# Performance work log

Hardware: AMD Instinct MI355X
Metric: run time of the kernel (lower is better)

Reference implementation:

```python
import jax, jax.numpy as jnp
import numpy as np

N_NODES = 10000
N_EDGES = 80000
IN_DIM, HID, OUT_DIM, HEADS = 768, 512, 768, 4
NEG_SLOPE = 0.2


def setup_inputs() -> dict:
    key = jax.random.key(0)
    ks = jax.random.split(key, 10)
    g = 0.05
    return {
        "x": jax.random.normal(ks[0], (N_NODES, IN_DIM), jnp.float32),
        "edge_index": jax.random.randint(ks[1], (2, N_EDGES), 0, N_NODES, jnp.int64),
        # layer 1: GATConv(768 -> 512, heads=4, concat=True)
        "W1": jax.random.normal(ks[2], (IN_DIM, HEADS * HID), jnp.float32) * g,
        "a1_src": jax.random.normal(ks[3], (HEADS, HID), jnp.float32) * g,
        "a1_dst": jax.random.normal(ks[4], (HEADS, HID), jnp.float32) * g,
        "b1": jnp.zeros((HEADS * HID,), jnp.float32),
        # layer 2: GATConv(2048 -> 768, heads=1, concat=False)
        "W2": jax.random.normal(ks[5], (HEADS * HID, OUT_DIM), jnp.float32) * g,
        "a2_src": jax.random.normal(ks[6], (1, OUT_DIM), jnp.float32) * g,
        "a2_dst": jax.random.normal(ks[7], (1, OUT_DIM), jnp.float32) * g,
        "b2": jnp.zeros((OUT_DIM,), jnp.float32),
    }


def _gat_layer(x, src, dst, W, a_src, a_dst, b, heads, d_out, concat):
    N = x.shape[0]
    h = (x @ W).reshape(N, heads, d_out)              # [N, H, D]
    as_n = jnp.einsum('nhd,hd->nh', h, a_src)          # [N, H]
    ad_n = jnp.einsum('nhd,hd->nh', h, a_dst)
    e = jax.nn.leaky_relu(as_n[src] + ad_n[dst], NEG_SLOPE)  # [E, H]
    # segment softmax over destination nodes
    e_max = jax.lax.stop_gradient(jax.ops.segment_max(e, dst, num_segments=N))
    ex = jnp.exp(e - e_max[dst])
    denom = jax.ops.segment_sum(ex, dst, num_segments=N)
    alpha = ex / (denom[dst] + 1e-16)                  # [E, H]
    msg = alpha[:, :, None] * h[src]                   # [E, H, D]
    out = jax.ops.segment_sum(msg, dst, num_segments=N)  # [N, H, D]
    out = out.reshape(N, heads * d_out) if concat else out.mean(axis=1)
    return out + b


def reference(x, edge_index, W1, a1_src, a1_dst, b1, W2, a2_src, a2_dst, b2):
    N = x.shape[0]
    # PyG GATConv default: add self-loops
    loops = jnp.arange(N, dtype=edge_index.dtype)
    src = jnp.concatenate([edge_index[0], loops])
    dst = jnp.concatenate([edge_index[1], loops])
    h = _gat_layer(x, src, dst, W1, a1_src, a1_dst, b1, HEADS, HID, True)
    h = jax.nn.elu(h)
    out = _gat_layer(h, src, dst, W2, a2_src, a2_dst, b2, 1, OUT_DIM, False)
    return out
```

## Files before the change

### kernel.cpp

```cpp
#include <hip/hip_runtime.h>
#include <hip/hip_bf16.h>

#define N_NODES 10000
#define E_REAL  80000
#define E_TOTAL 90000
#define IN_DIM  768
#define HID     512
#define HEADS   4
#define OUT_DIM 768
#define HD1     (HEADS * HID)
#define NEG_SLOPE 0.2f
#define H1_HSTRIDE (N_NODES * HID)

typedef unsigned short ushort_t;
typedef unsigned int uint_t;

__device__ inline float b2f(ushort_t u) { return __uint_as_float(((uint_t)u) << 16); }
__device__ inline ushort_t f2b(float f) {
    __hip_bfloat16 h = __float2bfloat16(f);
    return *reinterpret_cast<ushort_t*>(&h);
}

__device__ inline void edge_sd(const int* __restrict__ ei, int e, int& s, int& d) {
    if (e < E_REAL) { s = ei[e]; d = ei[E_REAL + e]; }
    else            { s = e - E_REAL; d = s; }
}

#define GLDS(g, l) __builtin_amdgcn_global_load_lds( \
    (const __attribute__((address_space(1))) void*)(g), \
    (__attribute__((address_space(3))) void*)(l), 16, 0, 0)

static const long B_H1B  = 0L;
static const long B_HB   = 40960000L;
static const long B_XB   = 81920000L;
static const long B_W1T  = 97280000L;
static const long B_W2T  = 100425728L;
static const long B_SM   = 103571456L;
static const long SM_AS1   = 0;
static const long SM_AD1   = 40000;
static const long SM_AS2   = 80000;
static const long SM_AD2   = 90000;
static const long SM_CNT   = 100000;
static const long SM_ROWS  = 110000;
static const long SM_CURS  = 120016;
static const long SM_END   = 130016;
static const long B_CSRS = B_SM + SM_END * 4;

__global__ __launch_bounds__(256)
void cast_bf16(const float* __restrict__ in, ushort_t* __restrict__ o, long n) {
    long i = ((long)blockIdx.x * 256 + threadIdx.x) * 8;
    if (i >= n) return;
    float4 v0 = *(const float4*)(in + i);
    float4 v1 = *(const float4*)(in + i + 4);
    ushort_t r[8] = {f2b(v0.x), f2b(v0.y), f2b(v0.z), f2b(v0.w),
                     f2b(v1.x), f2b(v1.y), f2b(v1.z), f2b(v1.w)};
    *(uint4*)(o + i) = *(uint4*)r;
}

__global__ __launch_bounds__(256)
void cast_transpose(const float* __restrict__ W, ushort_t* __restrict__ WT,
                    int K, int N) {
    __shared__ ushort_t t[32][33];
    const int n0 = blockIdx.x * 32, k0 = blockIdx.y * 32;
    const int tx = threadIdx.x & 31, ty = threadIdx.x >> 5;
#pragma unroll
    for (int i = 0; i < 4; ++i) {
        int k = ty + i * 8;
        t[k][tx] = f2b(W[(long)(k0 + k) * N + n0 + tx]);
    }
    __syncthreads();
#pragma unroll
    for (int i = 0; i < 4; ++i) {
        int n = ty + i * 8;
        WT[(long)(n0 + n) * K + k0 + tx] = t[tx][n];
    }
}

typedef short bf16x8 __attribute__((ext_vector_type(8)));
typedef float f32x4 __attribute__((ext_vector_type(4)));

#define GBM 256
#define GBN 128
#define GBK 64
#define ABUF (GBM * GBK)
#define BBUF (GBN * GBK)
#define GEMM_LDS_BYTES ((3 * (ABUF + BBUF)) * 2)

template<int CMODE>
__global__ __launch_bounds__(512)
void gemm8p(const ushort_t* __restrict__ A, const ushort_t* __restrict__ BT,
            ushort_t* __restrict__ C, int M, int N, int K) {
    extern __shared__ ushort_t sm_[];
    ushort_t* smA = sm_;
    ushort_t* smB = sm_ + 3 * ABUF;
    const int tid  = threadIdx.x;
    const int wave = tid >> 6, lane = tid & 63;
    const int quad = lane >> 4, l16 = lane & 15;
    const int bm = blockIdx.y * GBM, bn = blockIdx.x * GBN;
    const int wr = (wave >> 1) * 64, wc = (wave & 1) * 64;
    const int NT = K / GBK;

    const int  rA  = tid >> 3;
    const long cs8 = (long)(((tid & 7) ^ ((tid >> 3) & 7)) * 8);
    const ushort_t* aSrc = A  + (long)(bm + rA) * K + cs8;
    const ushort_t* bSrc = BT + (long)(bn + rA) * K + cs8;

    const int aRd  = (wr + l16) * GBK;
    const int bRd  = (wc + l16) * GBK;
    const int swz8 = l16 & 7;
    const int chq0 = ((quad)     ^ swz8) * 8;
    const int chq1 = ((4 + quad) ^ swz8) * 8;

    f32x4 acc[4][4] = {};

#pragma unroll
    for (int tt = 0; tt < 2; ++tt) {
        const long kt = (long)tt * GBK;
#pragma unroll
        for (int i = 0; i < 4; ++i)
            GLDS(aSrc + (long)i * 64 * K + kt,
                 smA + tt * ABUF + (i * 512 + wave * 64) * 8);
#pragma unroll
        for (int i = 0; i < 2; ++i)
            GLDS(bSrc + (long)i * 64 * K + kt,
                 smB + tt * BBUF + (i * 512 + wave * 64) * 8);
    }
    asm volatile("s_waitcnt vmcnt(6)" ::: "memory");
    __builtin_amdgcn_s_barrier();
    __builtin_amdgcn_sched_barrier(0);

    int bc = 0, bnx = 1, bs = 2;
    for (int t = 0; t < NT; ++t) {
        const int offA = bc * ABUF, offB = bc * BBUF;
        const bool stage = (t + 2 < NT);
        const long kt2 = (long)(t + 2) * GBK;
        bf16x8 bfr[2][4], af[2][2];

#pragma unroll
        for (int j = 0; j < 4; ++j) {
            bfr[0][j] = *(const bf16x8*)(smB + offB + bRd + j * 1024 + chq0);
            bfr[1][j] = *(const bf16x8*)(smB + offB + bRd + j * 1024 + chq1);
        }
#pragma unroll
        for (int ii = 0; ii < 2; ++ii) {
            af[0][ii] = *(const bf16x8*)(smA + offA + aRd + ii * 1024 + chq0);
            af[1][ii] = *(const bf16x8*)(smA + offA + aRd + ii * 1024 + chq1);
        }
        if (stage) {
            GLDS(aSrc + kt2,                    smA + bs * ABUF + (wave * 64) * 8);
            GLDS(aSrc + (long)1 * 64 * K + kt2, smA + bs * ABUF + (512 + wave * 64) * 8);
            GLDS(aSrc + (long)2 * 64 * K + kt2, smA + bs * ABUF + (1024 + wave * 64) * 8);
        }
        __builtin_amdgcn_sched_barrier(0);
        __builtin_amdgcn_s_barrier();
        __builtin_amdgcn_sched_barrier(0);
        __builtin_amdgcn_s_setprio(1);
#pragma unroll
        for (int kk = 0; kk < 2; ++kk)
#pragma unroll
            for (int ii = 0; ii < 2; ++ii)
#pragma unroll
                for (int j = 0; j < 4; ++j)
                    acc[ii][j] = __builtin_amdgcn_mfma_f32_16x16x32_bf16(
                        af[kk][ii], bfr[kk][j], acc[ii][j], 0, 0, 0);
        __builtin_amdgcn_s_setprio(0);
        __builtin_amdgcn_sched_barrier(0);
        __builtin_amdgcn_s_barrier();
        __builtin_amdgcn_sched_barrier(0);

#pragma unroll
        for (int ii = 0; ii < 2; ++ii) {
            af[0][ii] = *(const bf16x8*)(smA + offA + aRd + (2 + ii) * 1024 + chq0);
            af[1][ii] = *(const bf16x8*)(smA + offA + aRd + (2 + ii) * 1024 + chq1);
        }
        if (stage) {
            GLDS(aSrc + (long)3 * 64 * K + kt2, smA + bs * ABUF + (1536 + wave * 64) * 8);
            GLDS(bSrc + kt2,                    smB + bs * BBUF + (wave * 64) * 8);
            GLDS(bSrc + (long)1 * 64 * K + kt2, smB + bs * BBUF + (512 + wave * 64) * 8);
        }
        if (stage)             { asm volatile("s_waitcnt vmcnt(6)" ::: "memory"); }
        else if (t + 1 < NT)   { asm volatile("s_waitcnt vmcnt(0)" ::: "memory"); }
        __builtin_amdgcn_sched_barrier(0);
        __builtin_amdgcn_s_barrier();
        __builtin_amdgcn_sched_barrier(0);
        __builtin_amdgcn_s_setprio(1);
#pragma unroll
        for (int kk = 0; kk < 2; ++kk)
#pragma unroll
            for (int ii = 0; ii < 2; ++ii)
#pragma unroll
                for (int j = 0; j < 4; ++j)
                    acc[2 + ii][j] = __builtin_amdgcn_mfma_f32_16x16x32_bf16(
                        af[kk][ii], bfr[kk][j], acc[2 + ii][j], 0, 0, 0);
        __builtin_amdgcn_s_setprio(0);
        __builtin_amdgcn_sched_barrier(0);
        __builtin_amdgcn_s_barrier();
        __builtin_amdgcn_sched_barrier(0);

        int tmp = bc; bc = bnx; bnx = bs; bs = tmp;
    }

#pragma unroll
    for (int i = 0; i < 4; ++i) {
#pragma unroll
        for (int r = 0; r < 4; ++r) {
            int row = bm + wr + i * 16 + quad * 4 + r;
            if (row >= M) continue;
#pragma unroll
            for (int j = 0; j < 4; ++j) {
                int col = bn + wc + j * 16 + l16;
                if (CMODE == 0) {
                    C[(long)row * N + col] = f2b(acc[i][j][r]);
                } else {
                    C[(long)(col >> 9) * H1_HSTRIDE + (long)row * HID + (col & 511)]
                        = f2b(acc[i][j][r]);
                }
            }
        }
    }
}

__global__ __launch_bounds__(256)
void attn1(const ushort_t* __restrict__ h, const float* __restrict__ a_s,
           const float* __restrict__ a_d, float* __restrict__ os,
           float* __restrict__ od) {
    const int n = blockIdx.x;
    const int w = threadIdx.x >> 6, lane = threadIdx.x & 63;
    uint4 hv = *(const uint4*)(h + (long)w * H1_HSTRIDE + (long)n * HID + lane * 8);
    const float* asp = a_s + w * HID + lane * 8;
    const float* adp = a_d + w * HID + lane * 8;
    const ushort_t* pb = (const ushort_t*)&hv;
    float ps = 0.f, pd = 0.f;
#pragma unroll
    for (int c = 0; c < 8; ++c) {
        float v = b2f(pb[c]);
        ps += v * asp[c];
        pd += v * adp[c];
    }
#pragma unroll
    for (int off = 32; off > 0; off >>= 1) {
        ps += __shfl_down(ps, off);
        pd += __shfl_down(pd, off);
    }
    if (lane == 0) { os[n * HEADS + w] = ps; od[n * HEADS + w] = pd; }
}

__global__ __launch_bounds__(256)
void attn2(const ushort_t* __restrict__ h, const float* __restrict__ a_s,
           const float* __restrict__ a_d, float* __restrict__ os,
           float* __restrict__ od) {
    __shared__ float rs[4], rd[4];
    const int n = blockIdx.x, tid = threadIdx.x;
    const int w = tid >> 6, lane = tid & 63;
    float ps = 0.f, pd = 0.f;
#pragma unroll
    for (int j = 0; j < 3; ++j) {
        int c = tid + j * 256;
        float v = b2f(h[(long)n * OUT_DIM + c]);
        ps += v * a_s[c];
        pd += v * a_d[c];
    }
#pragma unroll
    for (int off = 32; off > 0; off >>= 1) {
        ps += __shfl_down(ps, off);
        pd += __shfl_down(pd, off);
    }
    if (lane == 0) { rs[w] = ps; rd[w] = pd; }
    __syncthreads();
    if (tid == 0) {
        os[n] = rs[0] + rs[1] + rs[2] + rs[3];
        od[n] = rd[0] + rd[1] + rd[2] + rd[3];
    }
}

__global__ __launch_bounds__(256)
void hist_dst(const int* __restrict__ ei, int* __restrict__ cnt) {
    int e = blockIdx.x * 256 + threadIdx.x;
    if (e >= E_TOTAL) return;
    int s, d; edge_sd(ei, e, s, d);
    atomicAdd(&cnt[d], 1);
}

#define SCAN_CH 40
__global__ __launch_bounds__(256)
void scan_nodes(const int* __restrict__ cnt, int* __restrict__ rows,
                int* __restrict__ curs) {
    __shared__ int part[256];
    const int tid = threadIdx.x;
    const int base = tid * SCAN_CH;
    int local[SCAN_CH];
    int sum = 0;
#pragma unroll
    for (int i = 0; i < SCAN_CH; ++i) {
        int idx = base + i;
        int v = (idx < N_NODES) ? cnt[idx] : 0;
        local[i] = v; sum += v;
    }
    part[tid] = sum;
    __syncthreads();
    for (int off = 1; off < 256; off <<= 1) {
        int v = (tid >= off) ? part[tid - off] : 0;
        __syncthreads();
        part[tid] += v;
        __syncthreads();
    }
    int run = part[tid] - sum;
#pragma unroll
    for (int i = 0; i < SCAN_CH; ++i) {
        int idx = base + i;
        if (idx < N_NODES) { rows[idx] = run; curs[idx] = run; run += local[i]; }
    }
    if (tid == 255) rows[N_NODES] = run;
}

__global__ __launch_bounds__(256)
void scatter_edges(const int* __restrict__ ei, int* __restrict__ curs,
                   int* __restrict__ csr_src) {
    int e = blockIdx.x * 256 + threadIdx.x;
    if (e >= E_TOTAL) return;
    int s, d; edge_sd(ei, e, s, d);
    int pos = atomicAdd(&curs[d], 1);
    csr_src[pos] = s;
}

__global__ __launch_bounds__(64)
void agg1(const int* __restrict__ rows, const int* __restrict__ csr_src,
          const float* __restrict__ as_n, const float* __restrict__ ad_n,
          const ushort_t* __restrict__ hf, const float* __restrict__ b1,
          ushort_t* __restrict__ o) {
    const int id = blockIdx.x;
    const int g = id & 7, j = id >> 3;
    const int hh = g >> 1;
    const int n = j * 2 + (g & 1);
    const int lane = threadIdx.x;
    const int beg = rows[n], end = rows[n + 1];
    const ushort_t* hsl = hf + (long)hh * H1_HSTRIDE;
    const float adv = ad_n[(long)n * HEADS + hh];
    float acc[8] = {};
    float dsum = 0.f;
    for (int k = beg; k < end; k += 4) {
        int nk = end - k; if (nk > 4) nk = 4;
        uint4 v[4]; float ex[4];
#pragma unroll
        for (int u = 0; u < 4; ++u) {
            if (u < nk) {
                int s = csr_src[k + u];
                float sc = as_n[(long)s * HEADS + hh] + adv;
                sc = sc > 0.f ? sc : NEG_SLOPE * sc;
                ex[u] = __expf(sc);
                v[u]  = *(const uint4*)(hsl + (long)s * HID + lane * 8);
            }
        }
#pragma unroll
        for (int u = 0; u < 4; ++u) {
            if (u < nk) {
                dsum += ex[u];
                const ushort_t* p = (const ushort_t*)&v[u];
#pragma unroll
                for (int c = 0; c < 8; ++c) acc[c] += ex[u] * b2f(p[c]);
            }
        }
    }
    const float dinv = 1.f / (dsum + 1e-16f);
    const float* bp = b1 + hh * HID + lane * 8;
    ushort_t r[8];
#pragma unroll
    for (int c = 0; c < 8; ++c) {
        float vv = acc[c] * dinv + bp[c];
        r[c] = f2b(vv > 0.f ? vv : expm1f(vv));
    }
    *(uint4*)(o + (long)n * HD1 + hh * HID + lane * 8) = *(uint4*)r;
}

#define PF2 8
__global__ __launch_bounds__(256)
void agg2(const int* __restrict__ rows, const int* __restrict__ csr_src,
          const float* __restrict__ as_n, const float* __restrict__ ad_n,
          const ushort_t* __restrict__ hf, const float* __restrict__ b2,
          float* __restrict__ out) {
    const int n = blockIdx.x * 4 + (threadIdx.x >> 6);
    const int lane = threadIdx.x & 63;
    const int beg = rows[n], end = rows[n + 1];
    const float adv = ad_n[n];
    float acc[12] = {};
    float dsum = 0.f;
    for (int k = beg; k < end; k += PF2) {
        int nk = end - k; if (nk > PF2) nk = PF2;
        int sv[PF2];
#pragma unroll
        for (int u = 0; u < PF2; ++u)
            if (u < nk) sv[u] = csr_src[k + u];
        uint4 v4[PF2]; uint2 v2[PF2]; float ex[PF2];
#pragma unroll
        for (int u = 0; u < PF2; ++u) {
            if (u < nk) {
                float sc = as_n[sv[u]] + adv;
                sc = sc > 0.f ? sc : NEG_SLOPE * sc;
                ex[u] = __expf(sc);
                const ushort_t* hp = hf + (long)sv[u] * OUT_DIM;
                v4[u] = *(const uint4*)(hp + lane * 8);
                v2[u] = *(const uint2*)(hp + 512 + lane * 4);
            }
        }
#pragma unroll
        for (int u = 0; u < PF2; ++u) {
            if (u < nk) {
                dsum += ex[u];
                const ushort_t* p4 = (const ushort_t*)&v4[u];
                const ushort_t* p2 = (const ushort_t*)&v2[u];
#pragma unroll
                for (int c = 0; c < 8; ++c) acc[c] += ex[u] * b2f(p4[c]);
#pragma unroll
                for (int c = 0; c < 4; ++c) acc[8 + c] += ex[u] * b2f(p2[c]);
            }
        }
    }
    const float dinv = 1.f / (dsum + 1e-16f);
    float* op = out + (long)n * OUT_DIM;
#pragma unroll
    for (int c = 0; c < 8; ++c)
        op[lane * 8 + c] = acc[c] * dinv + b2[lane * 8 + c];
#pragma unroll
    for (int c = 0; c < 4; ++c)
        op[512 + lane * 4 + c] = acc[8 + c] * dinv + b2[512 + lane * 4 + c];
}

extern "C" void kernel_launch(void* const* d_in, const int* in_sizes, int n_in,
                              void* d_out, int out_size, void* d_ws, size_t ws_size,
                              hipStream_t stream) {
    const float* x   = (const float*)d_in[0];
    const int*   ei  = (const int*)d_in[1];
    const float* W1  = (const float*)d_in[2];
    const float* a1s = (const float*)d_in[3];
    const float* a1d = (const float*)d_in[4];
    const float* b1  = (const float*)d_in[5];
    const float* W2  = (const float*)d_in[6];
    const float* a2s = (const float*)d_in[7];
    const float* a2d = (const float*)d_in[8];
    const float* b2  = (const float*)d_in[9];
    float* out = (float*)d_out;
    char* base = (char*)d_ws;

    ushort_t* h1b = (ushort_t*)(base + B_H1B);
    ushort_t* hb  = (ushort_t*)(base + B_HB);
    ushort_t* xb  = (ushort_t*)(base + B_XB);
    ushort_t* h2b = xb;
    ushort_t* w1t = (ushort_t*)(base + B_W1T);
    ushort_t* w2t = (ushort_t*)(base + B_W2T);
    float*    sm  = (float*)(base + B_SM);

    float* as1  = sm + SM_AS1;
    float* ad1  = sm + SM_AD1;
    float* as2  = sm + SM_AS2;
    float* ad2  = sm + SM_AD2;
    int* cnt    = (int*)(sm + SM_CNT);
    int* rows   = (int*)(sm + SM_ROWS);
    int* curs   = (int*)(sm + SM_CURS);
    int* csr_src = (int*)(base + B_CSRS);

    hipMemsetAsync(cnt, 0, 10000 * sizeof(int), stream);

    {
        long nx = (long)N_NODES * IN_DIM;
        cast_bf16<<<(int)(nx / 8 / 256 + 1), 256, 0, stream>>>(x, xb, nx);
        cast_transpose<<<dim3(HD1 / 32, IN_DIM / 32), 256, 0, stream>>>(W1, w1t, IN_DIM, HD1);
        cast_transpose<<<dim3(OUT_DIM / 32, HD1 / 32), 256, 0, stream>>>(W2, w2t, HD1, OUT_DIM);
        hist_dst<<<(E_TOTAL + 255) / 256, 256, 0, stream>>>(ei, cnt);
        scan_nodes<<<1, 256, 0, stream>>>(cnt, rows, curs);
        scatter_edges<<<(E_TOTAL + 255) / 256, 256, 0, stream>>>(ei, curs, csr_src);
    }

    gemm8p<1><<<dim3(HD1 / GBN, (N_NODES + GBM - 1) / GBM), 512, GEMM_LDS_BYTES, stream>>>(
        xb, w1t, h1b, N_NODES, HD1, IN_DIM);
    attn1<<<N_NODES, 256, 0, stream>>>(h1b, a1s, a1d, as1, ad1);
    agg1<<<N_NODES * HEADS, 64, 0, stream>>>(
        rows, csr_src, as1, ad1, h1b, b1, hb);

    gemm8p<0><<<dim3(OUT_DIM / GBN, (N_NODES + GBM - 1) / GBM), 512, GEMM_LDS_BYTES, stream>>>(
        hb, w2t, h2b, N_NODES, OUT_DIM, HD1);
    attn2<<<N_NODES, 256, 0, stream>>>(h2b, a2s, a2d, as2, ad2);
    agg2<<<N_NODES / 4, 256, 0, stream>>>(
        rows, csr_src, as2, ad2, h2b, b2, out);
}
```

Before: 326.5 us.

## Split layer-1 features into 256-wide slices and double agg1 parallelism

The layer-1 GEMM now writes its output as eight 256-column slices instead of four 512-column head planes. attn1 reads from the new layout, and agg1 launches one 64-thread block per node and slice, so each lane handles 4 features with 8-byte loads. The aim is more blocks in flight to hide gather latency, plus smaller contiguous gathers per slice. The cost is that every edge's score, exponential and index load are now computed twice per head, and each load is narrower.

After: 333.2 us. +2.0%, slower.

```diff
diff --git a/kernel.cpp b/kernel.cpp
--- a/kernel.cpp
+++ b/kernel.cpp
@@ -10,7 +10,7 @@
 #define OUT_DIM 768
 #define HD1     (HEADS * HID)
 #define NEG_SLOPE 0.2f
-#define H1_HSTRIDE (N_NODES * HID)
+#define S1_STRIDE (N_NODES * 256)
 
 typedef unsigned short ushort_t;
 typedef unsigned int uint_t;
@@ -212,7 +212,7 @@
                 if (CMODE == 0) {
                     C[(long)row * N + col] = f2b(acc[i][j][r]);
                 } else {
-                    C[(long)(col >> 9) * H1_HSTRIDE + (long)row * HID + (col & 511)]
+                    C[(long)(col >> 8) * S1_STRIDE + (long)row * 256 + (col & 255)]
                         = f2b(acc[i][j][r]);
                 }
             }
@@ -226,9 +226,11 @@
            float* __restrict__ od) {
     const int n = blockIdx.x;
     const int w = threadIdx.x >> 6, lane = threadIdx.x & 63;
-    uint4 hv = *(const uint4*)(h + (long)w * H1_HSTRIDE + (long)n * HID + lane * 8);
-    const float* asp = a_s + w * HID + lane * 8;
-    const float* adp = a_d + w * HID + lane * 8;
+    const int half = lane >> 5, l32 = lane & 31;
+    uint4 hv = *(const uint4*)(h + (long)(w * 2 + half) * S1_STRIDE
+                                 + (long)n * 256 + l32 * 8);
+    const float* asp = a_s + w * HID + half * 256 + l32 * 8;
+    const float* adp = a_d + w * HID + half * 256 + l32 * 8;
     const ushort_t* pb = (const ushort_t*)&hv;
     float ps = 0.f, pd = 0.f;
 #pragma unroll
@@ -329,18 +331,18 @@
           const ushort_t* __restrict__ hf, const float* __restrict__ b1,
           ushort_t* __restrict__ o) {
     const int id = blockIdx.x;
-    const int g = id & 7, j = id >> 3;
-    const int hh = g >> 1;
-    const int n = j * 2 + (g & 1);
+    const int slice = id & 7;
+    const int n = id >> 3;
+    const int hh = slice >> 1, half = slice & 1;
     const int lane = threadIdx.x;
     const int beg = rows[n], end = rows[n + 1];
-    const ushort_t* hsl = hf + (long)hh * H1_HSTRIDE;
+    const ushort_t* hsl = hf + (long)slice * S1_STRIDE;
     const float adv = ad_n[(long)n * HEADS + hh];
-    float acc[8] = {};
+    float acc[4] = {};
     float dsum = 0.f;
     for (int k = beg; k < end; k += 4) {
         int nk = end - k; if (nk > 4) nk = 4;
-        uint4 v[4]; float ex[4];
+        uint2 v[4]; float ex[4];
 #pragma unroll
         for (int u = 0; u < 4; ++u) {
             if (u < nk) {
@@ -348,7 +350,7 @@
                 float sc = as_n[(long)s * HEADS + hh] + adv;
                 sc = sc > 0.f ? sc : NEG_SLOPE * sc;
                 ex[u] = __expf(sc);
-                v[u]  = *(const uint4*)(hsl + (long)s * HID + lane * 8);
+                v[u]  = *(const uint2*)(hsl + (long)s * 256 + lane * 4);
             }
         }
 #pragma unroll
@@ -357,19 +359,19 @@
                 dsum += ex[u];
                 const ushort_t* p = (const ushort_t*)&v[u];
 #pragma unroll
-                for (int c = 0; c < 8; ++c) acc[c] += ex[u] * b2f(p[c]);
+                for (int c = 0; c < 4; ++c) acc[c] += ex[u] * b2f(p[c]);
             }
         }
     }
     const float dinv = 1.f / (dsum + 1e-16f);
-    const float* bp = b1 + hh * HID + lane * 8;
-    ushort_t r[8];
-#pragma unroll
-    for (int c = 0; c < 8; ++c) {
+    const float* bp = b1 + hh * HID + half * 256 + lane * 4;
+    ushort_t r[4];
+#pragma unroll
+    for (int c = 0; c < 4; ++c) {
         float vv = acc[c] * dinv + bp[c];
         r[c] = f2b(vv > 0.f ? vv : expm1f(vv));
     }
-    *(uint4*)(o + (long)n * HD1 + hh * HID + lane * 8) = *(uint4*)r;
+    *(uint2*)(o + (long)n * HD1 + hh * HID + half * 256 + lane * 4) = *(uint2*)r;
 }
 
 #define PF2 8
@@ -473,7 +475,7 @@
     gemm8p<1><<<dim3(HD1 / GBN, (N_NODES + GBM - 1) / GBM), 512, GEMM_LDS_BYTES, stream>>>(
         xb, w1t, h1b, N_NODES, HD1, IN_DIM);
     attn1<<<N_NODES, 256, 0, stream>>>(h1b, a1s, a1d, as1, ad1);
-    agg1<<<N_NODES * HEADS, 64, 0, stream>>>(
+    agg1<<<N_NODES * 8, 64, 0, stream>>>(
         rows, csr_src, as1, ad1, h1b, b1, hb);
 
     gemm8p<0><<<dim3(OUT_DIM / GBN, (N_NODES + GBM - 1) / GBM), 512, GEMM_LDS_BYTES, stream>>>(
```
